# Performance work log

Hardware: AMD Instinct MI355X
Metric: run time of the kernel (lower is better)

Reference implementation:

```python
import jax, jax.numpy as jnp
import numpy as np

B, N, IN_F, H, OUT_F = 8, 2048, 128, 4, 32
ALPHA = 0.2  # LeakyReLU negative slope


def setup_inputs() -> dict:
    key = jax.random.key(0)
    k1, k2, k3, k4, k5 = jax.random.split(key, 5)
    x = jax.random.normal(k1, (B, N, IN_F), dtype=jnp.float32)
    adj = jax.random.randint(k2, (N, N), 0, 2, dtype=jnp.int32)
    # add self-loops so no row is fully masked (avoids all -inf softmax rows)
    adj = adj.at[jnp.arange(N), jnp.arange(N)].set(1)
    W = jax.random.normal(k3, (H, IN_F, OUT_F), dtype=jnp.float32) * 0.1
    a_src = jax.random.normal(k4, (H, OUT_F, 1), dtype=jnp.float32) * 0.1
    a_dst = jax.random.normal(k5, (H, OUT_F, 1), dtype=jnp.float32) * 0.1
    return {"x": x, "adj": adj, "W": W, "a_src": a_src, "a_dst": a_dst}


def reference(x, adj, W, a_src, a_dst):
    # h: (B,H,N,O)
    h = jnp.einsum('bni,hio->bhno', x, W)
    # additive attention logits
    e_src = jnp.einsum('bhno,ho->bhn', h, a_src[..., 0])  # (B,H,N)
    e_dst = jnp.einsum('bhno,ho->bhn', h, a_dst[..., 0])  # (B,H,N)
    e = e_src[:, :, :, None] + e_dst[:, :, None, :]       # (B,H,N,N)
    e = jnp.where(e > 0, e, ALPHA * e)                    # leaky_relu
    mask = (adj != 0)[None, None, :, :]                   # (1,1,N,N), broadcast over B,H
    e = jnp.where(mask, e, -jnp.inf)
    attention = jax.nn.softmax(e, axis=-1)
    attention = jnp.where(mask, attention, 0.0)           # zero out masked (inf) entries
    # dropout is identity in eval mode
    h_prime = jnp.einsum('bhnm,bhmo->bhno', attention, h)  # (B,H,N,O)
    # concat heads: (B,N,H*O)
    out = h_prime.transpose(0, 2, 1, 3).reshape(B, N, H * OUT_F)
    return out
```

## Files before the change

kernel.cpp:

```cpp
#include <hip/hip_runtime.h>
#include <stdint.h>

#define B_    8
#define N_    2048
#define INF_  128
#define H_    4
#define OUTF_ 32
#define BH_   (B_*H_)
#define ALPHA_ 0.2f

typedef __attribute__((ext_vector_type(8))) short bf16x8;
typedef __attribute__((ext_vector_type(4))) short bf16x4;
typedef __attribute__((ext_vector_type(4))) float f32x4;

static __device__ __forceinline__ short bf16_rne(float f) {
  uint32_t u = __float_as_uint(f);
  u += 0x7fffu + ((u >> 16) & 1u);
  return (short)(u >> 16);
}
#define BF16_SPLIT(f, dsthi, dstlo) {                         \
    const float f_ = (f);                                     \
    const uint32_t uh_ = __float_as_uint(f_) & 0xffff0000u;   \
    (dsthi) = (short)(uh_ >> 16);                             \
    (dstlo) = bf16_rne(f_ - __uint_as_float(uh_)); }


__global__ void k_wt(const float* __restrict__ W, short* __restrict__ WThi,
                     short* __restrict__ WTlo) {
  const int h = blockIdx.x, k = threadIdx.x;
#pragma unroll
  for (int c = 0; c < OUTF_; ++c) {
    short hi, lo;
    BF16_SPLIT(W[(h * INF_ + k) * OUTF_ + c], hi, lo);
    WThi[(h * OUTF_ + c) * INF_ + k] = hi;
    WTlo[(h * OUTF_ + c) * INF_ + k] = lo;
  }
}

__global__ __launch_bounds__(256) void k_pack_adj(const int* __restrict__ adj,
                                                  unsigned long long* __restrict__ bits) {
  const int i = blockIdx.x;
  const int t = threadIdx.x;
  const int* row = adj + (size_t)i * N_;
#pragma unroll
  for (int it = 0; it < N_ / 256; ++it) {
    const int j = it * 256 + t;
    const unsigned long long m = __ballot(row[j] != 0);
    if ((t & 63) == 0) bits[(size_t)i * (N_ / 64) + it * 4 + (t >> 6)] = m;
  }
}

__global__ __launch_bounds__(256) void k_feat(const float* __restrict__ x,
    const short* __restrict__ WThi, const short* __restrict__ WTlo,
    const float* __restrict__ asrc, const float* __restrict__ adst,
    short* __restrict__ hThi, short* __restrict__ hTlo,
    float* __restrict__ Aarr, float* __restrict__ Barr, float* __restrict__ nsarr,
    float* __restrict__ darr, float* __restrict__ uarr, float* __restrict__ varr)
{
  const int t = threadIdx.x, lane = t & 63, wv = t >> 6;
  const int blk = blockIdx.x, bh = blk >> 5, itile = blk & 31;
  const int b = bh >> 2, hh = bh & 3;
  const int i0 = itile * 64 + wv * 16;
  const int cl = lane & 15, g = lane >> 4;

  const float* xr   = x + ((size_t)b * N_ + i0 + cl) * INF_ + g * 8;
  const size_t wo0 = (size_t)(hh * OUTF_ + cl) * INF_ + g * 8;
  const size_t wo1 = (size_t)(hh * OUTF_ + 16 + cl) * INF_ + g * 8;

  f32x4 acc0 = {0.f, 0.f, 0.f, 0.f}, acc1 = {0.f, 0.f, 0.f, 0.f};
#pragma unroll
  for (int kt = 0; kt < 4; ++kt) {
    const int kb = kt * 32;
    const f32x4 xa = *(const f32x4*)(xr + kb);
    const f32x4 xb = *(const f32x4*)(xr + kb + 4);
    bf16x8 ah, al;
    BF16_SPLIT(xa[0], ah[0], al[0]); BF16_SPLIT(xa[1], ah[1], al[1]);
    BF16_SPLIT(xa[2], ah[2], al[2]); BF16_SPLIT(xa[3], ah[3], al[3]);
    BF16_SPLIT(xb[0], ah[4], al[4]); BF16_SPLIT(xb[1], ah[5], al[5]);
    BF16_SPLIT(xb[2], ah[6], al[6]); BF16_SPLIT(xb[3], ah[7], al[7]);
    const bf16x8 b0h = *(const bf16x8*)(WThi + wo0 + kb);
    const bf16x8 b0l = *(const bf16x8*)(WTlo + wo0 + kb);
    const bf16x8 b1h = *(const bf16x8*)(WThi + wo1 + kb);
    const bf16x8 b1l = *(const bf16x8*)(WTlo + wo1 + kb);
    acc0 = __builtin_amdgcn_mfma_f32_16x16x32_bf16(ah, b0h, acc0, 0, 0, 0);
    acc0 = __builtin_amdgcn_mfma_f32_16x16x32_bf16(al, b0h, acc0, 0, 0, 0);
    acc0 = __builtin_amdgcn_mfma_f32_16x16x32_bf16(ah, b0l, acc0, 0, 0, 0);
    acc1 = __builtin_amdgcn_mfma_f32_16x16x32_bf16(ah, b1h, acc1, 0, 0, 0);
    acc1 = __builtin_amdgcn_mfma_f32_16x16x32_bf16(al, b1h, acc1, 0, 0, 0);
    acc1 = __builtin_amdgcn_mfma_f32_16x16x32_bf16(ah, b1l, acc1, 0, 0, 0);
  }

  bf16x4 h0h, h0l, h1h, h1l;
  BF16_SPLIT(acc0[0], h0h[0], h0l[0]); BF16_SPLIT(acc0[1], h0h[1], h0l[1]);
  BF16_SPLIT(acc0[2], h0h[2], h0l[2]); BF16_SPLIT(acc0[3], h0h[3], h0l[3]);
  BF16_SPLIT(acc1[0], h1h[0], h1l[0]); BF16_SPLIT(acc1[1], h1h[1], h1l[1]);
  BF16_SPLIT(acc1[2], h1h[2], h1l[2]); BF16_SPLIT(acc1[3], h1h[3], h1l[3]);
  const size_t jw = (size_t)i0 + g * 4;
  const size_t c0 = ((size_t)bh * OUTF_ + cl) * N_ + jw;
  const size_t c1 = ((size_t)bh * OUTF_ + 16 + cl) * N_ + jw;
  *(bf16x4*)(hThi + c0) = h0h;
  *(bf16x4*)(hTlo + c0) = h0l;
  *(bf16x4*)(hThi + c1) = h1h;
  *(bf16x4*)(hTlo + c1) = h1l;

  const float as0 = asrc[hh * OUTF_ + cl], as1 = asrc[hh * OUTF_ + 16 + cl];
  const float ad0 = adst[hh * OUTF_ + cl], ad1 = adst[hh * OUTF_ + 16 + cl];
  float es0 = acc0[0] * as0 + acc1[0] * as1;
  float es1 = acc0[1] * as0 + acc1[1] * as1;
  float es2 = acc0[2] * as0 + acc1[2] * as1;
  float es3 = acc0[3] * as0 + acc1[3] * as1;
  float ed0 = acc0[0] * ad0 + acc1[0] * ad1;
  float ed1 = acc0[1] * ad0 + acc1[1] * ad1;
  float ed2 = acc0[2] * ad0 + acc1[2] * ad1;
  float ed3 = acc0[3] * ad0 + acc1[3] * ad1;
#pragma unroll
  for (int m = 1; m <= 8; m <<= 1) {
    es0 += __shfl_xor(es0, m); es1 += __shfl_xor(es1, m);
    es2 += __shfl_xor(es2, m); es3 += __shfl_xor(es3, m);
    ed0 += __shfl_xor(ed0, m); ed1 += __shfl_xor(ed1, m);
    ed2 += __shfl_xor(ed2, m); ed3 += __shfl_xor(ed3, m);
  }
  if (cl < 4) {
    const float s  = cl == 0 ? es0 : cl == 1 ? es1 : cl == 2 ? es2 : es3;
    const float dd = cl == 0 ? ed0 : cl == 1 ? ed1 : cl == 2 ? ed2 : ed3;
    const size_t ri = (size_t)bh * N_ + i0 + g * 4 + cl;
    Aarr[ri]  = expf(s);
    Barr[ri]  = expf(ALPHA_ * s);
    nsarr[ri] = -s;
    darr[ri]  = dd;
    uarr[ri]  = expf(dd);
    varr[ri]  = expf(ALPHA_ * dd);
  }
}

#define TILE_DUV_ 4096
#define TILE_MSK_ 4480
#define TILE_SZ_  4736

__global__ __launch_bounds__(256, 4) void k_attn(const short* __restrict__ hThi,
    const short* __restrict__ hTlo, const uint32_t* __restrict__ bits32,
    const float* __restrict__ Aarr, const float* __restrict__ Barr,
    const float* __restrict__ nsarr, const float* __restrict__ darr,
    const float* __restrict__ uarr, const float* __restrict__ varr,
    float* __restrict__ out)
{
  __shared__ __align__(16) char smem[2][TILE_SZ_];

  const int t = threadIdx.x, lane = t & 63, wv = t >> 6;
  const int blk = blockIdx.x, bh = blk >> 5, itile = blk & 31;
  const int b = bh >> 2, hh = bh & 3;
  const int i0b = itile * 64;
  const int i0 = i0b + wv * 16;
  const int cl = lane & 15, g = lane >> 4;
  const int jb = g * 8;

  const size_t rbase = (size_t)bh * N_;
  const float Ai  = Aarr[rbase + i0 + cl];
  const float Bi  = Barr[rbase + i0 + cl];
  const float nsi = nsarr[rbase + i0 + cl];

  const int sc = t >> 3, ss = t & 7;
  const short* hsrc = (ss < 4 ? hThi + ss * 8 : hTlo + (ss - 4) * 8)
                      + ((size_t)bh * OUTF_ + sc) * N_;
  const int h_dst = sc * 128 + ((ss * 16) ^ ((sc & 7) << 4));
  const float* duvsrc = (t < 8 ? darr : (t < 16 ? uarr : varr)) + rbase + (t & 7) * 4;
  const uint32_t* msksrc = bits32 + (size_t)(i0b + (t & 63)) * (N_ / 32);

  const int swz = (cl & 7) << 4;
  const int off_h0h = cl * 128 + ((g * 16) ^ swz);
  const int off_h0l = cl * 128 + ((64 + g * 16) ^ swz);
  const int off_h1h = (16 + cl) * 128 + ((g * 16) ^ swz);
  const int off_h1l = (16 + cl) * 128 + ((64 + g * 16) ^ swz);
  const int off_d0 = TILE_DUV_ + g * 32,       off_d1 = off_d0 + 16;
  const int off_u0 = TILE_DUV_ + 128 + g * 32, off_u1 = off_u0 + 16;
  const int off_v0 = TILE_DUV_ + 256 + g * 32, off_v1 = off_v0 + 16;
  const int off_m  = TILE_MSK_ + (wv * 16 + cl) * 4;

  f32x4 acc0 = {0.f, 0.f, 0.f, 0.f}, acc1 = {0.f, 0.f, 0.f, 0.f};
  float z = 0.f;
  bf16x8 sth; f32x4 stduv; uint32_t stmsk;

#define STAGE_LOAD(JT) {                                        \
    sth = *(const bf16x8*)(hsrc + (JT) * 32);                   \
    if (t < 24) stduv = *(const f32x4*)(duvsrc + (JT) * 32);    \
    if (t >= 64 && t < 128) stmsk = msksrc[(JT)]; }

#define STAGE_WRITE(BI) {                                                   \
    char* sb_ = smem[BI];                                                   \
    *(bf16x8*)(sb_ + h_dst) = sth;                                          \
    if (t < 24) *(f32x4*)(sb_ + TILE_DUV_ + t * 16) = stduv;                \
    if (t >= 64 && t < 128) *(uint32_t*)(sb_ + TILE_MSK_ + (t - 64) * 4) = stmsk; }

#define WGEN(E, DE, UE, VE) {                                   \
    const bool c_ = (DE) > nsi;                                 \
    float w_ = (c_ ? Ai : Bi) * (c_ ? (UE) : (VE));             \
    w_ = ((wsh >> (E)) & 1u) ? w_ : 0.f;                        \
    const uint32_t hi_ = __float_as_uint(w_) & 0xffff0000u;     \
    whi[E] = (short)(hi_ >> 16);                                \
    wlo[E] = (short)(__float_as_uint(w_ - __uint_as_float(hi_)) >> 16); \
    z += w_; }

#define COMPUTE(BI) {                                                 \
    const char* sb_ = smem[BI];                                       \
    const f32x4 d0 = *(const f32x4*)(sb_ + off_d0);                   \
    const f32x4 d1 = *(const f32x4*)(sb_ + off_d1);                   \
    const f32x4 u0 = *(const f32x4*)(sb_ + off_u0);                   \
    const f32x4 u1 = *(const f32x4*)(sb_ + off_u1);                   \
    const f32x4 v0 = *(const f32x4*)(sb_ + off_v0);                   \
    const f32x4 v1 = *(const f32x4*)(sb_ + off_v1);                   \
    const bf16x8 h0h = *(const bf16x8*)(sb_ + off_h0h);               \
    const bf16x8 h0l = *(const bf16x8*)(sb_ + off_h0l);               \
    const bf16x8 h1h = *(const bf16x8*)(sb_ + off_h1h);               \
    const bf16x8 h1l = *(const bf16x8*)(sb_ + off_h1l);               \
    const uint32_t wsh = (*(const uint32_t*)(sb_ + off_m)) >> jb;     \
    bf16x8 whi, wlo;                                                  \
    WGEN(0, d0[0], u0[0], v0[0])                                      \
    WGEN(1, d0[1], u0[1], v0[1])                                      \
    WGEN(2, d0[2], u0[2], v0[2])                                      \
    WGEN(3, d0[3], u0[3], v0[3])                                      \
    WGEN(4, d1[0], u1[0], v1[0])                                      \
    WGEN(5, d1[1], u1[1], v1[1])                                      \
    WGEN(6, d1[2], u1[2], v1[2])                                      \
    WGEN(7, d1[3], u1[3], v1[3])                                      \
    acc0 = __builtin_amdgcn_mfma_f32_16x16x32_bf16(whi, h0h, acc0, 0, 0, 0); \
    acc0 = __builtin_amdgcn_mfma_f32_16x16x32_bf16(wlo, h0h, acc0, 0, 0, 0); \
    acc0 = __builtin_amdgcn_mfma_f32_16x16x32_bf16(whi, h0l, acc0, 0, 0, 0); \
    acc1 = __builtin_amdgcn_mfma_f32_16x16x32_bf16(whi, h1h, acc1, 0, 0, 0); \
    acc1 = __builtin_amdgcn_mfma_f32_16x16x32_bf16(wlo, h1h, acc1, 0, 0, 0); \
    acc1 = __builtin_amdgcn_mfma_f32_16x16x32_bf16(whi, h1l, acc1, 0, 0, 0); }

  STAGE_LOAD(0)
  STAGE_WRITE(0)
  __syncthreads();
#pragma unroll 1
  for (int jt = 0; jt < N_ / 32; jt += 2) {
    STAGE_LOAD(jt + 1)
    COMPUTE(0)
    STAGE_WRITE(1)
    __syncthreads();
    if (jt + 2 < N_ / 32) STAGE_LOAD(jt + 2)
    COMPUTE(1)
    if (jt + 2 < N_ / 32) STAGE_WRITE(0)
    __syncthreads();
  }
#undef COMPUTE
#undef WGEN
#undef STAGE_WRITE
#undef STAGE_LOAD

  z += __shfl_xor(z, 16);
  z += __shfl_xor(z, 32);

  float* op = out + ((size_t)b * N_ + i0) * (H_ * OUTF_) + hh * OUTF_;
#pragma unroll
  for (int q = 0; q < 4; ++q) {
    const float zr = __shfl(z, g * 4 + q);
    const float inv = 1.0f / zr;
    op[(size_t)(g * 4 + q) * (H_ * OUTF_) + cl]      = acc0[q] * inv;
    op[(size_t)(g * 4 + q) * (H_ * OUTF_) + 16 + cl] = acc1[q] * inv;
  }
}

extern "C" void kernel_launch(void* const* d_in, const int* in_sizes, int n_in,
                              void* d_out, int out_size, void* d_ws, size_t ws_size,
                              hipStream_t stream) {
  const float* x    = (const float*)d_in[0];
  const int*   adj  = (const int*)d_in[1];
  const float* W    = (const float*)d_in[2];
  const float* asrc = (const float*)d_in[3];
  const float* adst = (const float*)d_in[4];
  float* out = (float*)d_out;

  char* ws = (char*)d_ws;
  short* hThi = (short*)ws;
  short* hTlo = (short*)(ws + 4194304);
  unsigned long long* bits = (unsigned long long*)(ws + 8388608);
  float* Aarr  = (float*)(ws + 8912896);
  float* Barr  = Aarr  + BH_ * N_;
  float* nsarr = Barr  + BH_ * N_;
  float* darr  = nsarr + BH_ * N_;
  float* uarr  = darr  + BH_ * N_;
  float* varr  = uarr  + BH_ * N_;
  short* WThi  = (short*)(ws + 10485760);
  short* WTlo  = (short*)(ws + 10518528);

  hipLaunchKernelGGL(k_wt, dim3(H_), dim3(INF_), 0, stream, W, WThi, WTlo);
  hipLaunchKernelGGL(k_pack_adj, dim3(N_), dim3(256), 0, stream, adj, bits);
  hipLaunchKernelGGL(k_feat, dim3(BH_ * 32), dim3(256), 0, stream,
                     x, WThi, WTlo, asrc, adst, hThi, hTlo,
                     Aarr, Barr, nsarr, darr, uarr, varr);
  hipLaunchKernelGGL(k_attn, dim3(BH_ * 32), dim3(256), 0, stream,
                     hThi, hTlo, (const uint32_t*)bits,
                     Aarr, Barr, nsarr, darr, uarr, varr, out);
}
```

Baseline: 149.3 us.

## Factor per-row exp scales out of weights and compute denominators with MFMA

The per-element attention weight A_i*u_j or B_i*v_j is split into two masked selections of precomputed bf16 hi/lo u and v values, accumulated in separate MFMA accumulators. The row scales A_i and B_i are applied once in the epilogue, and the softmax denominator comes from MFMAs against a ones vector instead of scalar adds and shuffles. This replaces per-element float multiplies and bf16 splitting with bitwise masking, but doubles the MFMA count (from 6 to 16 per tile) and adds accumulator registers. The u/v split now happens once per tile during the shared-memory write.

```diff
diff --git a/kernel.cpp b/kernel.cpp
--- a/kernel.cpp
+++ b/kernel.cpp
@@ -12,6 +12,7 @@
 typedef __attribute__((ext_vector_type(8))) short bf16x8;
 typedef __attribute__((ext_vector_type(4))) short bf16x4;
 typedef __attribute__((ext_vector_type(4))) float f32x4;
+typedef __attribute__((ext_vector_type(4))) unsigned int u32x4;
 
 static __device__ __forceinline__ short bf16_rne(float f) {
   uint32_t u = __float_as_uint(f);
@@ -133,9 +134,13 @@
   }
 }
 
-#define TILE_DUV_ 4096
+#define TILE_D_   4096
+#define TILE_U_   4224
+#define TILE_V_   4352
 #define TILE_MSK_ 4480
 #define TILE_SZ_  4736
+
+#define MF(a, bb, c) __builtin_amdgcn_mfma_f32_16x16x32_bf16(a, bb, c, 0, 0, 0)
 
 __global__ __launch_bounds__(256, 4) void k_attn(const short* __restrict__ hThi,
     const short* __restrict__ hTlo, const uint32_t* __restrict__ bits32,
@@ -171,13 +176,17 @@
   const int off_h0l = cl * 128 + ((64 + g * 16) ^ swz);
   const int off_h1h = (16 + cl) * 128 + ((g * 16) ^ swz);
   const int off_h1l = (16 + cl) * 128 + ((64 + g * 16) ^ swz);
-  const int off_d0 = TILE_DUV_ + g * 32,       off_d1 = off_d0 + 16;
-  const int off_u0 = TILE_DUV_ + 128 + g * 32, off_u1 = off_u0 + 16;
-  const int off_v0 = TILE_DUV_ + 256 + g * 32, off_v1 = off_v0 + 16;
+  const int off_d0 = TILE_D_ + g * 32, off_d1 = off_d0 + 16;
+  const int off_uh = TILE_U_ + g * 16, off_ul = TILE_U_ + 64 + g * 16;
+  const int off_vh = TILE_V_ + g * 16, off_vl = TILE_V_ + 64 + g * 16;
   const int off_m  = TILE_MSK_ + (wv * 16 + cl) * 4;
 
-  f32x4 acc0 = {0.f, 0.f, 0.f, 0.f}, acc1 = {0.f, 0.f, 0.f, 0.f};
-  float z = 0.f;
+  const short one_ = (short)0x3F80;
+  const bf16x8 ONESF = {one_, one_, one_, one_, one_, one_, one_, one_};
+
+  f32x4 accu0 = {0.f,0.f,0.f,0.f}, accu1 = {0.f,0.f,0.f,0.f};
+  f32x4 accv0 = {0.f,0.f,0.f,0.f}, accv1 = {0.f,0.f,0.f,0.f};
+  f32x4 acczu = {0.f,0.f,0.f,0.f}, acczv = {0.f,0.f,0.f,0.f};
   bf16x8 sth; f32x4 stduv; uint32_t stmsk;
 
 #define STAGE_LOAD(JT) {                                        \
@@ -188,46 +197,57 @@
 #define STAGE_WRITE(BI) {                                                   \
     char* sb_ = smem[BI];                                                   \
     *(bf16x8*)(sb_ + h_dst) = sth;                                          \
-    if (t < 24) *(f32x4*)(sb_ + TILE_DUV_ + t * 16) = stduv;                \
+    if (t < 8) { *(f32x4*)(sb_ + TILE_D_ + t * 16) = stduv; }               \
+    else if (t < 24) {                                                      \
+      bf16x4 sh_, sl_;                                                      \
+      BF16_SPLIT(stduv[0], sh_[0], sl_[0]);                                 \
+      BF16_SPLIT(stduv[1], sh_[1], sl_[1]);                                 \
+      BF16_SPLIT(stduv[2], sh_[2], sl_[2]);                                 \
+      BF16_SPLIT(stduv[3], sh_[3], sl_[3]);                                 \
+      const int base_ = (t < 16) ? TILE_U_ : TILE_V_;                       \
+      const int sl8_ = (t & 7) * 8;                                         \
+      *(bf16x4*)(sb_ + base_ + sl8_)      = sh_;                            \
+      *(bf16x4*)(sb_ + base_ + 64 + sl8_) = sl_;                            \
+    }                                                                       \
     if (t >= 64 && t < 128) *(uint32_t*)(sb_ + TILE_MSK_ + (t - 64) * 4) = stmsk; }
 
-#define WGEN(E, DE, UE, VE) {                                   \
-    const bool c_ = (DE) > nsi;                                 \
-    float w_ = (c_ ? Ai : Bi) * (c_ ? (UE) : (VE));             \
-    w_ = ((wsh >> (E)) & 1u) ? w_ : 0.f;                        \
-    const uint32_t hi_ = __float_as_uint(w_) & 0xffff0000u;     \
-    whi[E] = (short)(hi_ >> 16);                                \
-    wlo[E] = (short)(__float_as_uint(w_ - __uint_as_float(hi_)) >> 16); \
-    z += w_; }
+#define MPAIR(P, DA, DB) {                                                  \
+    const bool cA_ = (DA) > nsi, cB_ = (DB) > nsi;                          \
+    const bool bA_ = (wsh >> (2 * (P))) & 1u;                               \
+    const bool bB_ = (wsh >> (2 * (P) + 1)) & 1u;                           \
+    const uint32_t m1_ = ((cA_ && bA_) ? 0xFFFFu : 0u) |                    \
+                         ((cB_ && bB_) ? 0xFFFF0000u : 0u);                 \
+    const uint32_t m2_ = ((!cA_ && bA_) ? 0xFFFFu : 0u) |                   \
+                         ((!cB_ && bB_) ? 0xFFFF0000u : 0u);                \
+    p1h[P] = uhw[P] & m1_; p1l[P] = ulw[P] & m1_;                           \
+    p2h[P] = vhw[P] & m2_; p2l[P] = vlw[P] & m2_; }
 
 #define COMPUTE(BI) {                                                 \
     const char* sb_ = smem[BI];                                       \
     const f32x4 d0 = *(const f32x4*)(sb_ + off_d0);                   \
     const f32x4 d1 = *(const f32x4*)(sb_ + off_d1);                   \
-    const f32x4 u0 = *(const f32x4*)(sb_ + off_u0);                   \
-    const f32x4 u1 = *(const f32x4*)(sb_ + off_u1);                   \
-    const f32x4 v0 = *(const f32x4*)(sb_ + off_v0);                   \
-    const f32x4 v1 = *(const f32x4*)(sb_ + off_v1);                   \
     const bf16x8 h0h = *(const bf16x8*)(sb_ + off_h0h);               \
     const bf16x8 h0l = *(const bf16x8*)(sb_ + off_h0l);               \
     const bf16x8 h1h = *(const bf16x8*)(sb_ + off_h1h);               \
     const bf16x8 h1l = *(const bf16x8*)(sb_ + off_h1l);               \
+    const u32x4 uhw = *(const u32x4*)(sb_ + off_uh);                  \
+    const u32x4 ulw = *(const u32x4*)(sb_ + off_ul);                  \
+    const u32x4 vhw = *(const u32x4*)(sb_ + off_vh);                  \
+    const u32x4 vlw = *(const u32x4*)(sb_ + off_vl);                  \
     const uint32_t wsh = (*(const uint32_t*)(sb_ + off_m)) >> jb;     \
-    bf16x8 whi, wlo;                                                  \
-    WGEN(0, d0[0], u0[0], v0[0])                                      \
-    WGEN(1, d0[1], u0[1], v0[1])                                      \
-    WGEN(2, d0[2], u0[2], v0[2])                                      \
-    WGEN(3, d0[3], u0[3], v0[3])                                      \
-    WGEN(4, d1[0], u1[0], v1[0])                                      \
-    WGEN(5, d1[1], u1[1], v1[1])                                      \
-    WGEN(6, d1[2], u1[2], v1[2])                                      \
-    WGEN(7, d1[3], u1[3], v1[3])                                      \
-    acc0 = __builtin_amdgcn_mfma_f32_16x16x32_bf16(whi, h0h, acc0, 0, 0, 0); \
-    acc0 = __builtin_amdgcn_mfma_f32_16x16x32_bf16(wlo, h0h, acc0, 0, 0, 0); \
-    acc0 = __builtin_amdgcn_mfma_f32_16x16x32_bf16(whi, h0l, acc0, 0, 0, 0); \
-    acc1 = __builtin_amdgcn_mfma_f32_16x16x32_bf16(whi, h1h, acc1, 0, 0, 0); \
-    acc1 = __builtin_amdgcn_mfma_f32_16x16x32_bf16(wlo, h1h, acc1, 0, 0, 0); \
-    acc1 = __builtin_amdgcn_mfma_f32_16x16x32_bf16(whi, h1l, acc1, 0, 0, 0); }
+    u32x4 p1h, p1l, p2h, p2l;                                         \
+    MPAIR(0, d0[0], d0[1]) MPAIR(1, d0[2], d0[3])                     \
+    MPAIR(2, d1[0], d1[1]) MPAIR(3, d1[2], d1[3])                     \
+    const bf16x8 A1h = __builtin_bit_cast(bf16x8, p1h);               \
+    const bf16x8 A1l = __builtin_bit_cast(bf16x8, p1l);               \
+    const bf16x8 A2h = __builtin_bit_cast(bf16x8, p2h);               \
+    const bf16x8 A2l = __builtin_bit_cast(bf16x8, p2l);               \
+    accu0 = MF(A1h, h0h, accu0); accu0 = MF(A1l, h0h, accu0); accu0 = MF(A1h, h0l, accu0); \
+    accu1 = MF(A1h, h1h, accu1); accu1 = MF(A1l, h1h, accu1); accu1 = MF(A1h, h1l, accu1); \
+    accv0 = MF(A2h, h0h, accv0); accv0 = MF(A2l, h0h, accv0); accv0 = MF(A2h, h0l, accv0); \
+    accv1 = MF(A2h, h1h, accv1); accv1 = MF(A2l, h1h, accv1); accv1 = MF(A2h, h1l, accv1); \
+    acczu = MF(A1h, ONESF, acczu); acczu = MF(A1l, ONESF, acczu);     \
+    acczv = MF(A2h, ONESF, acczv); acczv = MF(A2l, ONESF, acczv); }
 
   STAGE_LOAD(0)
   STAGE_WRITE(0)
@@ -244,20 +264,20 @@
     __syncthreads();
   }
 #undef COMPUTE
-#undef WGEN
+#undef MPAIR
 #undef STAGE_WRITE
 #undef STAGE_LOAD
 
-  z += __shfl_xor(z, 16);
-  z += __shfl_xor(z, 32);
-
   float* op = out + ((size_t)b * N_ + i0) * (H_ * OUTF_) + hh * OUTF_;
 #pragma unroll
   for (int q = 0; q < 4; ++q) {
-    const float zr = __shfl(z, g * 4 + q);
-    const float inv = 1.0f / zr;
-    op[(size_t)(g * 4 + q) * (H_ * OUTF_) + cl]      = acc0[q] * inv;
-    op[(size_t)(g * 4 + q) * (H_ * OUTF_) + 16 + cl] = acc1[q] * inv;
+    const int row = g * 4 + q;
+    const float Ar = __shfl(Ai, row);
+    const float Br = __shfl(Bi, row);
+    const float Zr = Ar * acczu[q] + Br * acczv[q];
+    const float inv = 1.0f / Zr;
+    op[(size_t)row * (H_ * OUTF_) + cl]      = (Ar * accu0[q] + Br * accv0[q]) * inv;
+    op[(size_t)row * (H_ * OUTF_) + 16 + cl] = (Ar * accu1[q] + Br * accv1[q]) * inv;
   }
 }
 
```

After: 160.3 us. +7.4%, slower.
